# Kernel tuning notes

Hardware: AMD Instinct MI355X
Metric: run time of the kernel (lower is better)

Reference implementation:

```python
import jax, jax.numpy as jnp
import numpy as np

EPS = 1e-5
NEG_SLOPE = 0.1


def conv_bn_lrelu(x, w, g, b, rm, rv):
    # 1x1 conv (no bias) + BatchNorm (inference, running stats) + LeakyReLU(0.1)
    # x: [B,C,H,W], w: [O,C]
    y = jnp.einsum('bchw,oc->bohw', x, w)
    scale = g / jnp.sqrt(rv + EPS)
    y = y * scale[None, :, None, None] + (b - rm * scale)[None, :, None, None]
    return jnp.where(y >= 0, y, NEG_SLOPE * y)


def setup_inputs() -> dict:
    key = jax.random.key(0)
    ks = jax.random.split(key, 16)
    B, C, H1, W1, H2, W2 = 4, 256, 32, 32, 64, 64
    C8 = C // 8
    inp = {
        'x1': jax.random.normal(ks[0], (B, C, H1, W1), jnp.float32),
        'x2': jax.random.normal(ks[1], (B, C, H2, W2), jnp.float32),
        'wq': jax.random.normal(ks[2], (C8, C), jnp.float32) * 0.05,
        'wk': jax.random.normal(ks[3], (C8, C), jnp.float32) * 0.05,
        'wv': jax.random.normal(ks[4], (C, C), jnp.float32) * 0.05,
        'gq': jnp.ones((C8,), jnp.float32), 'bq': jnp.zeros((C8,), jnp.float32),
        'mq': jax.random.normal(ks[5], (C8,), jnp.float32) * 0.1,
        'vq': jax.random.uniform(ks[6], (C8,), jnp.float32, 0.5, 1.5),
        'gk': jnp.ones((C8,), jnp.float32), 'bk': jnp.zeros((C8,), jnp.float32),
        'mk': jax.random.normal(ks[7], (C8,), jnp.float32) * 0.1,
        'vk': jax.random.uniform(ks[8], (C8,), jnp.float32, 0.5, 1.5),
        'gv': jnp.ones((C,), jnp.float32), 'bv': jnp.zeros((C,), jnp.float32),
        'mv': jax.random.normal(ks[9], (C,), jnp.float32) * 0.1,
        'vv': jax.random.uniform(ks[10], (C,), jnp.float32, 0.5, 1.5),
        'gamma': jnp.full((1,), 0.5, jnp.float32),
    }
    return inp


def reference(x1, x2, wq, wk, wv, gq, bq, mq, vq, gk, bk, mk, vk, gv, bv, mv, vv, gamma):
    B, C, H2, W2 = x2.shape
    # bilinear upsample x1 to x2's spatial size (align_corners=False == half-pixel)
    x1u = jax.image.resize(x1, (B, C, H2, W2), method='bilinear')
    N = H2 * W2
    q = conv_bn_lrelu(x1u, wq, gq, bq, mq, vq).reshape(B, -1, N)  # [B,C8,N]
    k = conv_bn_lrelu(x2, wk, gk, bk, mk, vk).reshape(B, -1, N)   # [B,C8,N]
    v = conv_bn_lrelu(x2, wv, gv, bv, mv, vv).reshape(B, -1, N)   # [B,C,N]
    energy = jnp.einsum('bdm,bdn->bmn', q, k)                      # [B,N,N]
    attn = jax.nn.softmax(energy, axis=-1)
    out = jnp.einsum('bcn,bmn->bcm', v, attn).reshape(B, C, H2, W2)
    return gamma[0] * out + x1u
```

## Files before the change

### kernel.cpp

```cpp
#include <hip/hip_runtime.h>

#define B_ 4
#define C_ 256
#define N_ 4096
#define LOG2E 1.4426950408889634f

typedef short short8 __attribute__((ext_vector_type(8)));
typedef short short4_ __attribute__((ext_vector_type(4)));
typedef float float4v __attribute__((ext_vector_type(4)));
typedef unsigned int uint2v __attribute__((ext_vector_type(2)));
typedef unsigned int u32;

__device__ inline unsigned short f2b(float x){
  unsigned u = __builtin_bit_cast(unsigned, x);
  u = u + 0x7FFFu + ((u >> 16) & 1u);
  return (unsigned short)(u >> 16);
}
__device__ inline float b2f(unsigned short s){
  return __builtin_bit_cast(float, ((u32)s) << 16);
}
__device__ inline u32 cvtpk(float lo, float hi){
  u32 r; asm("v_cvt_pk_bf16_f32 %0, %1, %2" : "=v"(r) : "v"(lo), "v"(hi)); return r;
}
__device__ inline void gload16(const void* g, void* l){
  __builtin_amdgcn_global_load_lds((const __attribute__((address_space(1))) u32*)g,
                                   (__attribute__((address_space(3))) u32*)l, 16, 0, 0);
}

__global__ void fold_w_kernel(const float* __restrict__ wq, const float* __restrict__ wk,
    const float* __restrict__ wv,
    const float* gq, const float* bq, const float* mq, const float* vq,
    const float* gk, const float* bk, const float* mk, const float* vk,
    const float* gv, const float* bv, const float* mv, const float* vv,
    unsigned short* wqb, unsigned short* wkb, unsigned short* wvb,
    float* biasq, float* biask, float* biasv){
  int i = blockIdx.x*256 + threadIdx.x;
  int o = i >> 8;
  float sv = gv[o]*rsqrtf(vv[o]+1e-5f);
  wvb[i] = f2b(wv[i]*sv);
  if (i < 32*256){
    int oq = i >> 8;
    float sq = gq[oq]*rsqrtf(vq[oq]+1e-5f);
    wqb[i] = f2b(wq[i]*sq*LOG2E);
    float sk = gk[oq]*rsqrtf(vk[oq]+1e-5f);
    wkb[i] = f2b(wk[i]*sk);
  }
  if (i < 256) biasv[i] = bv[i] - mv[i]*(gv[i]*rsqrtf(vv[i]+1e-5f));
  if (i < 32){
    biasq[i] = (bq[i] - mq[i]*(gq[i]*rsqrtf(vq[i]+1e-5f)))*LOG2E;
    biask[i] = bk[i] - mk[i]*(gk[i]*rsqrtf(vk[i]+1e-5f));
  }
}

__global__ __launch_bounds__(256, 2)
void pre_kernel(const float* __restrict__ x1, const float* __restrict__ x2,
                const unsigned short* __restrict__ wqb,
                const unsigned short* __restrict__ wkb,
                const unsigned short* __restrict__ wvb,
                const float* __restrict__ biasq, const float* __restrict__ biask,
                const float* __restrict__ biasv,
                unsigned short* __restrict__ Qb, unsigned short* __restrict__ Kb,
                unsigned short* __restrict__ Vb){
  __shared__ unsigned short xt[64*260];
  int b = blockIdx.y;
  int t = threadIdx.x;
  int lane = t&63, w = t>>6, l15 = lane&15, g = lane>>4;

  if (blockIdx.z == 0){
    int y = blockIdx.x;
    float fy = 0.5f*y - 0.25f;
    float y0f = floorf(fy); float wy = fy - y0f;
    int y0 = max(0,min(31,(int)y0f)), y1 = max(0,min(31,(int)y0f+1));
    int x = t & 63, cg = t >> 6;
    float fx = 0.5f*x - 0.25f;
    float x0f = floorf(fx); float wx = fx - x0f;
    int x0 = max(0,min(31,(int)x0f)), x1i = max(0,min(31,(int)x0f+1));
    #pragma unroll 8
    for (int i=0;i<64;i++){
      int c = cg + i*4;
      const float* s0 = x1 + ((size_t)(b*C_ + c)*32 + y0)*32;
      const float* s1 = x1 + ((size_t)(b*C_ + c)*32 + y1)*32;
      float v00=s0[x0], v01=s0[x1i], v10=s1[x0], v11=s1[x1i];
      float v0 = v00 + wx*(v01-v00), v1 = v10 + wx*(v11-v10);
      float val = v0 + wy*(v1-v0);
      xt[x*260 + c] = f2b(val);
    }
    __syncthreads();
    const unsigned short* arow = xt + (w*16+l15)*260 + g*8;
    short8 a[8];
    #pragma unroll
    for (int kk=0;kk<8;kk++){
      short4_ lo = *(const short4_*)(arow + kk*32);
      short4_ hi = *(const short4_*)(arow + kk*32 + 4);
      short8 af;
      af[0]=lo[0];af[1]=lo[1];af[2]=lo[2];af[3]=lo[3];
      af[4]=hi[0];af[5]=hi[1];af[6]=hi[2];af[7]=hi[3];
      a[kk]=af;
    }
    #pragma unroll
    for (int ot=0; ot<2; ot++){
      int o = ot*16 + l15;
      const unsigned short* wrow = wqb + o*C_ + g*8;
      float4v acc = {0.f,0.f,0.f,0.f};
      #pragma unroll
      for (int kk=0;kk<8;kk++){
        short8 bf = *(const short8*)(wrow + kk*32);
        acc = __builtin_amdgcn_mfma_f32_16x16x32_bf16(a[kk], bf, acc, 0,0,0);
      }
      float bs = biasq[o];
      #pragma unroll
      for (int r=0;r<4;r++){
        float yv = acc[r] + bs;
        yv = yv >= 0.f ? yv : 0.1f*yv;
        int m = y*64 + w*16 + g*4 + r;
        Qb[(size_t)(b*N_+m)*32 + o] = f2b(yv);
      }
    }
  } else {
    int n0 = blockIdx.x*64;
    int n = t & 63, cg = t >> 6;
    #pragma unroll 8
    for (int i=0;i<64;i++){
      int c = cg + i*4;
      float v = x2[(size_t)(b*C_ + c)*N_ + n0 + n];
      xt[n*260 + c] = f2b(v);
    }
    __syncthreads();
    const unsigned short* arow = xt + (w*16+l15)*260 + g*8;
    short8 a[8];
    #pragma unroll
    for (int kk=0;kk<8;kk++){
      short4_ lo = *(const short4_*)(arow + kk*32);
      short4_ hi = *(const short4_*)(arow + kk*32 + 4);
      short8 af;
      af[0]=lo[0];af[1]=lo[1];af[2]=lo[2];af[3]=lo[3];
      af[4]=hi[0];af[5]=hi[1];af[6]=hi[2];af[7]=hi[3];
      a[kk]=af;
    }
    if (blockIdx.z == 1){
      #pragma unroll
      for (int ot=0; ot<2; ot++){
        int o = ot*16 + l15;
        const unsigned short* wrow = wkb + o*C_ + g*8;
        float4v acc = {0.f,0.f,0.f,0.f};
        #pragma unroll
        for (int kk=0;kk<8;kk++){
          short8 bf = *(const short8*)(wrow + kk*32);
          acc = __builtin_amdgcn_mfma_f32_16x16x32_bf16(a[kk], bf, acc, 0,0,0);
        }
        float bs = biask[o];
        #pragma unroll
        for (int r=0;r<4;r++){
          float yv = acc[r] + bs;
          yv = yv >= 0.f ? yv : 0.1f*yv;
          int m = n0 + w*16 + g*4 + r;
          Kb[(size_t)(b*N_+m)*32 + o] = f2b(yv);
        }
      }
    }
    int obase = (blockIdx.z == 1) ? 0 : 8;
    #pragma unroll
    for (int ot=0; ot<8; ot++){
      int o = (obase + ot)*16 + l15;
      const unsigned short* wrow = wvb + (size_t)o*C_ + g*8;
      float4v acc = {0.f,0.f,0.f,0.f};
      #pragma unroll
      for (int kk=0;kk<8;kk++){
        short8 bf = *(const short8*)(wrow + kk*32);
        acc = __builtin_amdgcn_mfma_f32_16x16x32_bf16(a[kk], bf, acc, 0,0,0);
      }
      float bs = biasv[o];
      #pragma unroll
      for (int r=0;r<4;r++){
        float yv = acc[r] + bs;
        yv = yv >= 0.f ? yv : 0.1f*yv;
        int m = n0 + w*16 + g*4 + r;
        Vb[(size_t)(b*C_ + o)*N_ + m] = f2b(yv);
      }
    }
  }
}

__global__ __launch_bounds__(512, 2)
void attn_kernel(const unsigned short* __restrict__ Qb,
                 const unsigned short* __restrict__ Kb,
                 const unsigned short* __restrict__ Vb,
                 unsigned short* __restrict__ partial,
                 float* __restrict__ statsg){
  __shared__ __align__(16) char smem[43552];
  int* flagsB = (int*)(smem + 43008);
  float* sclB = (float*)(smem + 43040);

  int wg = (blockIdx.z*4 + blockIdx.y)*64 + blockIdx.x;
  int id = (wg & 7)*64 + (wg >> 3);
  int ng = id >> 8, b = (id >> 6) & 3, mblk = id & 63;
  int t = threadIdx.x, lane = t & 63, w = t >> 6;
  int l15 = lane & 15, g = lane >> 4;

  short8 qf{};
  if (w < 4)
    qf = *(const short8*)(Qb + (size_t)(b*N_ + mblk*64 + w*16 + l15)*32 + g*8);

  float4v acc[4][2];
  #pragma unroll
  for (int mt=0;mt<4;mt++)
    #pragma unroll
    for (int ct=0;ct<2;ct++) acc[mt][ct] = (float4v){0.f,0.f,0.f,0.f};
  float mrow = -1e30f, lrun = 0.f;
  const float4v zero4 = {0.f,0.f,0.f,0.f};

  u32 goff[2]; int loff[2];
  #pragma unroll
  for (int j=0;j<2;j++){
    int i = j*512 + t;
    int c = i >> 2, jj = i & 3;
    loff[j] = i*16;
    goff[j] = (u32)(c*(N_*2)) + (u32)((jj ^ (c & 3)) << 4);
  }
  const char* Vbyte = (const char*)Vb + (size_t)b*C_*N_*2 + ng*4096;
  const short* kbase = (const short*)Kb + (size_t)(b*N_ + ng*2048 + l15)*32 + g*8;

  auto stageV = [&](int tt, int par){
    const char* src = Vbyte + tt*64;
    #pragma unroll
    for (int j=0;j<2;j++) gload16(src + goff[j], smem + par*16384 + loff[j]);
  };
  auto loadK = [&](short8 (&kf)[2], int tt){
    const short* kp = kbase + (size_t)tt*1024;
    #pragma unroll
    for (int j=0;j<2;j++) kf[j] = *(const short8*)(kp + j*512);
  };

  auto softmax_step = [&](const short8 (&kf)[2], int pdst){
    float4v s[2];
    #pragma unroll
    for (int j=0;j<2;j++)
      s[j] = __builtin_amdgcn_mfma_f32_16x16x32_bf16(kf[j], qf, zero4, 0, 0, 0);
    float tmax = fmaxf(fmaxf(fmaxf(s[0][0],s[0][1]),fmaxf(s[0][2],s[0][3])),
                       fmaxf(fmaxf(s[1][0],s[1][1]),fmaxf(s[1][2],s[1][3])));
    int trig = __any((tmax > mrow + 8.f) ? 1 : 0) ? 1 : 0;
    if (lane == 0) flagsB[pdst*4 + w] = trig;
    if (trig){
      float tm = fmaxf(tmax, __shfl_xor(tmax, 16));
      tm = fmaxf(tm, __shfl_xor(tm, 32));
      float mnew = fmaxf(mrow, tm);
      float sc = exp2f(mrow - mnew);
      mrow = mnew; lrun *= sc;
      if (lane < 16) sclB[pdst*64 + w*16 + l15] = sc;
    }
    char* pw = smem + 32768 + pdst*5120 + w*1280 + l15*80;
    #pragma unroll
    for (int j=0;j<2;j++){
      float p0 = exp2f(s[j][0]-mrow), p1 = exp2f(s[j][1]-mrow);
      float p2 = exp2f(s[j][2]-mrow), p3 = exp2f(s[j][3]-mrow);
      lrun += (p0+p1)+(p2+p3);
      u32 lo = cvtpk(p0, p1);
      u32 hi = cvtpk(p2, p3);
      *(uint2v*)(pw + j*32 + g*8) = (uint2v){lo, hi};
    }
  };

  auto body = [&](int tt, short8 (&kC)[2], short8 (&kN)[2]){
    int pp = tt & 1, nx = (tt+1) & 1;
    if (tt < 63) stageV(tt+1, nx);
    if (w < 4){
      loadK(kN, (tt+2) & 63);
      if (tt < 63) softmax_step(kC, nx);
    }
    #pragma unroll
    for (int mt=0;mt<4;mt++){
      if (flagsB[pp*4 + mt]){
        float4v sv = *(float4v*)(sclB + pp*64 + mt*16 + g*4);
        #pragma unroll
        for (int ct=0;ct<2;ct++){
          acc[mt][ct][0]*=sv[0]; acc[mt][ct][1]*=sv[1];
          acc[mt][ct][2]*=sv[2]; acc[mt][ct][3]*=sv[3];
        }
      }
    }
    const char* pb = smem + 32768 + pp*5120;
    const char* vbc = smem + pp*16384;
    short8 pa[4], vf[2];
    #pragma unroll
    for (int mt=0;mt<4;mt++)
      pa[mt] = *(const short8*)(pb + mt*1280 + l15*80 + g*16);
    #pragma unroll
    for (int ct=0;ct<2;ct++){
      int row = w*32 + ct*16 + l15;
      vf[ct] = *(const short8*)(vbc + row*64 + ((g*16) ^ ((row & 3) << 4)));
    }
    __builtin_amdgcn_s_setprio(1);
    #pragma unroll
    for (int mt=0;mt<4;mt++)
      #pragma unroll
      for (int ct=0;ct<2;ct++)
        acc[mt][ct] = __builtin_amdgcn_mfma_f32_16x16x32_bf16(pa[mt], vf[ct], acc[mt][ct], 0, 0, 0);
    __builtin_amdgcn_s_setprio(0);
    __syncthreads();
  };

  short8 kA[2], kB[2];
  stageV(0, 0);
  if (w < 4){
    short8 k0[2];
    loadK(k0, 0);
    softmax_step(k0, 0);
    loadK(kA, 1);
  }
  __syncthreads();

  for (int tt=0; tt<64; tt+=2){
    body(tt,   kA, kB);
    body(tt+1, kB, kA);
  }

  if (w < 4){
    lrun += __shfl_xor(lrun, 16);
    lrun += __shfl_xor(lrun, 32);
    if (lane < 16){
      int sidx = (((b*2+ng)*64 + mblk)*64 + w*16 + l15)*2;
      statsg[sidx] = mrow; statsg[sidx+1] = lrun;
    }
  }
  size_t pbg = (size_t)((b*2+ng)*64 + mblk)*16384;
  #pragma unroll
  for (int mt=0;mt<4;mt++)
    #pragma unroll
    for (int ct=0;ct<2;ct++)
      #pragma unroll
      for (int r=0;r<4;r++){
        int m = mt*16 + g*4 + r;
        int c = w*32 + ct*16 + l15;
        partial[pbg + m*256 + c] = f2b(acc[mt][ct][r]);
      }
}

__global__ __launch_bounds__(256, 2)
void combine_kernel(const unsigned short* __restrict__ partial,
                    const float* __restrict__ statsg,
                    const float* __restrict__ x1,
                    const float* __restrict__ gamma_p,
                    float* __restrict__ out){
  __shared__ float tile[64][65];
  __shared__ float fbuf[64][3];
  int b = blockIdx.z, mblk = blockIdx.y, ct4 = blockIdx.x;
  int t = threadIdx.x;
  float gm = gamma_p[0];
  if (t < 64){
    int s0 = (((b*2+0)*64 + mblk)*64 + t)*2;
    int s1 = (((b*2+1)*64 + mblk)*64 + t)*2;
    float m0 = statsg[s0], l0 = statsg[s0+1];
    float m1 = statsg[s1], l1 = statsg[s1+1];
    float M = fmaxf(m0, m1);
    float f0 = exp2f(m0 - M), f1 = exp2f(m1 - M);
    float L = l0*f0 + l1*f1;
    fbuf[t][0] = f0; fbuf[t][1] = f1; fbuf[t][2] = gm / L;
  }
  __syncthreads();
  size_t p0b = (size_t)((b*2+0)*64 + mblk)*16384 + ct4*64;
  size_t p1b = (size_t)((b*2+1)*64 + mblk)*16384 + ct4*64;
  int c_l = t & 63, mg = t >> 6;
  #pragma unroll 4
  for (int pass=0; pass<16; pass++){
    int m = pass*4 + mg;
    float v0 = b2f(partial[p0b + m*256 + c_l]);
    float v1 = b2f(partial[p1b + m*256 + c_l]);
    tile[m][c_l] = (v0*fbuf[m][0] + v1*fbuf[m][1]) * fbuf[m][2];
  }
  __syncthreads();
  int y = mblk;
  float fy = 0.5f*y - 0.25f;
  float y0f = floorf(fy); float wy = fy - y0f;
  int y0 = max(0,min(31,(int)y0f)), y1 = max(0,min(31,(int)y0f+1));
  int m = t & 63, cg = t >> 6;
  float fx = 0.5f*m - 0.25f;
  float x0f = floorf(fx); float wx = fx - x0f;
  int x0 = max(0,min(31,(int)x0f)), x1i = max(0,min(31,(int)x0f+1));
  #pragma unroll 4
  for (int pass=0; pass<16; pass++){
    int c_l2 = pass*4 + cg;
    const float* s0 = x1 + ((size_t)(b*C_ + ct4*64 + c_l2)*32 + y0)*32;
    const float* s1 = x1 + ((size_t)(b*C_ + ct4*64 + c_l2)*32 + y1)*32;
    float v00=s0[x0], v01=s0[x1i], v10=s1[x0], v11=s1[x1i];
    float v0 = v00 + wx*(v01-v00), v1 = v10 + wx*(v11-v10);
    float xv = v0 + wy*(v1-v0);
    size_t gidx = ((size_t)(b*C_ + ct4*64 + c_l2))*N_ + mblk*64 + m;
    out[gidx] = tile[m][c_l2] + xv;
  }
}

extern "C" void kernel_launch(void* const* d_in, const int* in_sizes, int n_in,
                              void* d_out, int out_size, void* d_ws, size_t ws_size,
                              hipStream_t stream){
  (void)in_sizes; (void)n_in; (void)out_size; (void)ws_size;
  const float* x1 = (const float*)d_in[0];
  const float* x2 = (const float*)d_in[1];
  const float* wq = (const float*)d_in[2];
  const float* wk = (const float*)d_in[3];
  const float* wv = (const float*)d_in[4];
  const float* gq = (const float*)d_in[5];
  const float* bq = (const float*)d_in[6];
  const float* mq = (const float*)d_in[7];
  const float* vq = (const float*)d_in[8];
  const float* gk = (const float*)d_in[9];
  const float* bk = (const float*)d_in[10];
  const float* mk = (const float*)d_in[11];
  const float* vk = (const float*)d_in[12];
  const float* gv = (const float*)d_in[13];
  const float* bv = (const float*)d_in[14];
  const float* mv = (const float*)d_in[15];
  const float* vv = (const float*)d_in[16];
  const float* gamma = (const float*)d_in[17];
  float* out = (float*)d_out;

  char* p = (char*)d_ws;
  unsigned short* Qb    = (unsigned short*)p; p += (size_t)B_*N_*32*2;
  unsigned short* Kb    = (unsigned short*)p; p += (size_t)B_*N_*32*2;
  unsigned short* Vb    = (unsigned short*)p; p += (size_t)B_*C_*N_*2;
  unsigned short* wqb   = (unsigned short*)p; p += 32*256*2;
  unsigned short* wkb   = (unsigned short*)p; p += 32*256*2;
  unsigned short* wvb   = (unsigned short*)p; p += 256*256*2;
  float* biasq          = (float*)p;          p += 32*4;
  float* biask          = (float*)p;          p += 32*4;
  float* biasv          = (float*)p;          p += 256*4;
  unsigned short* parti = (unsigned short*)p; p += (size_t)512*16384*2;
  float* statsg         = (float*)p;          p += (size_t)512*64*2*4;

  fold_w_kernel<<<256, 256, 0, stream>>>(wq,wk,wv,gq,bq,mq,vq,gk,bk,mk,vk,gv,bv,mv,vv,
                                         wqb,wkb,wvb,biasq,biask,biasv);
  pre_kernel<<<dim3(64,4,3), 256, 0, stream>>>(x1, x2, wqb, wkb, wvb,
                                               biasq, biask, biasv, Qb, Kb, Vb);
  attn_kernel<<<dim3(64,4,2), 512, 0, stream>>>(Qb, Kb, Vb, parti, statsg);
  combine_kernel<<<dim3(4,64,4), 256, 0, stream>>>(parti, statsg, x1, gamma, out);
}
```

Before: 110.3 us.

## Split attention key dimension four ways and strengthen V LDS swizzle

Attention now splits the N keys into four chunks instead of two, launching 1024 workgroups that each process 32 key tiles. The combine kernel merges four partial softmax states. This gives more parallelism on a 256-CU device and shortens each block's serial loop. The cost is twice the partial-output traffic and a heavier combine step. The LDS swizzle for V tiles also XORs in an extra row bit to reduce bank conflicts.

```diff
diff --git a/kernel.cpp b/kernel.cpp
--- a/kernel.cpp
+++ b/kernel.cpp
@@ -192,7 +192,7 @@
   float* sclB = (float*)(smem + 43040);
 
   int wg = (blockIdx.z*4 + blockIdx.y)*64 + blockIdx.x;
-  int id = (wg & 7)*64 + (wg >> 3);
+  int id = (wg & 7)*128 + (wg >> 3);
   int ng = id >> 8, b = (id >> 6) & 3, mblk = id & 63;
   int t = threadIdx.x, lane = t & 63, w = t >> 6;
   int l15 = lane & 15, g = lane >> 4;
@@ -213,12 +213,13 @@
   #pragma unroll
   for (int j=0;j<2;j++){
     int i = j*512 + t;
-    int c = i >> 2, jj = i & 3;
+    int c = i >> 2, sp = i & 3;
+    int jj = sp ^ (c & 3) ^ ((c >> 2) & 3);
     loff[j] = i*16;
-    goff[j] = (u32)(c*(N_*2)) + (u32)((jj ^ (c & 3)) << 4);
-  }
-  const char* Vbyte = (const char*)Vb + (size_t)b*C_*N_*2 + ng*4096;
-  const short* kbase = (const short*)Kb + (size_t)(b*N_ + ng*2048 + l15)*32 + g*8;
+    goff[j] = (u32)(c*(N_*2)) + (u32)(jj << 4);
+  }
+  const char* Vbyte = (const char*)Vb + (size_t)b*C_*N_*2 + ng*2048;
+  const short* kbase = (const short*)Kb + (size_t)(b*N_ + ng*1024 + l15)*32 + g*8;
 
   auto stageV = [&](int tt, int par){
     const char* src = Vbyte + tt*64;
@@ -262,10 +263,10 @@
 
   auto body = [&](int tt, short8 (&kC)[2], short8 (&kN)[2]){
     int pp = tt & 1, nx = (tt+1) & 1;
-    if (tt < 63) stageV(tt+1, nx);
+    if (tt < 31) stageV(tt+1, nx);
     if (w < 4){
-      loadK(kN, (tt+2) & 63);
-      if (tt < 63) softmax_step(kC, nx);
+      loadK(kN, (tt+2) & 31);
+      if (tt < 31) softmax_step(kC, nx);
     }
     #pragma unroll
     for (int mt=0;mt<4;mt++){
@@ -287,7 +288,8 @@
     #pragma unroll
     for (int ct=0;ct<2;ct++){
       int row = w*32 + ct*16 + l15;
-      vf[ct] = *(const short8*)(vbc + row*64 + ((g*16) ^ ((row & 3) << 4)));
+      int slot = g ^ (row & 3) ^ ((row >> 2) & 3);
+      vf[ct] = *(const short8*)(vbc + row*64 + slot*16);
     }
     __builtin_amdgcn_s_setprio(1);
     #pragma unroll
@@ -309,7 +311,7 @@
   }
   __syncthreads();
 
-  for (int tt=0; tt<64; tt+=2){
+  for (int tt=0; tt<32; tt+=2){
     body(tt,   kA, kB);
     body(tt+1, kB, kA);
   }
@@ -318,11 +320,11 @@
     lrun += __shfl_xor(lrun, 16);
     lrun += __shfl_xor(lrun, 32);
     if (lane < 16){
-      int sidx = (((b*2+ng)*64 + mblk)*64 + w*16 + l15)*2;
+      int sidx = (((b*4+ng)*64 + mblk)*64 + w*16 + l15)*2;
       statsg[sidx] = mrow; statsg[sidx+1] = lrun;
     }
   }
-  size_t pbg = (size_t)((b*2+ng)*64 + mblk)*16384;
+  size_t pbg = (size_t)((b*4+ng)*64 + mblk)*16384;
   #pragma unroll
   for (int mt=0;mt<4;mt++)
     #pragma unroll
@@ -342,30 +344,41 @@
                     const float* __restrict__ gamma_p,
                     float* __restrict__ out){
   __shared__ float tile[64][65];
-  __shared__ float fbuf[64][3];
+  __shared__ float fbuf[64][5];
   int b = blockIdx.z, mblk = blockIdx.y, ct4 = blockIdx.x;
   int t = threadIdx.x;
   float gm = gamma_p[0];
   if (t < 64){
-    int s0 = (((b*2+0)*64 + mblk)*64 + t)*2;
-    int s1 = (((b*2+1)*64 + mblk)*64 + t)*2;
-    float m0 = statsg[s0], l0 = statsg[s0+1];
-    float m1 = statsg[s1], l1 = statsg[s1+1];
-    float M = fmaxf(m0, m1);
-    float f0 = exp2f(m0 - M), f1 = exp2f(m1 - M);
-    float L = l0*f0 + l1*f1;
-    fbuf[t][0] = f0; fbuf[t][1] = f1; fbuf[t][2] = gm / L;
+    float mq[4], lq[4];
+    #pragma unroll
+    for (int q=0;q<4;q++){
+      int s = (((b*4+q)*64 + mblk)*64 + t)*2;
+      mq[q] = statsg[s]; lq[q] = statsg[s+1];
+    }
+    float M = fmaxf(fmaxf(mq[0],mq[1]), fmaxf(mq[2],mq[3]));
+    float L = 0.f;
+    #pragma unroll
+    for (int q=0;q<4;q++){
+      float f = exp2f(mq[q] - M);
+      fbuf[t][q] = f;
+      L += lq[q]*f;
+    }
+    fbuf[t][4] = gm / L;
   }
   __syncthreads();
-  size_t p0b = (size_t)((b*2+0)*64 + mblk)*16384 + ct4*64;
-  size_t p1b = (size_t)((b*2+1)*64 + mblk)*16384 + ct4*64;
+  size_t pqb[4];
+  #pragma unroll
+  for (int q=0;q<4;q++)
+    pqb[q] = (size_t)((b*4+q)*64 + mblk)*16384 + ct4*64;
   int c_l = t & 63, mg = t >> 6;
   #pragma unroll 4
   for (int pass=0; pass<16; pass++){
     int m = pass*4 + mg;
-    float v0 = b2f(partial[p0b + m*256 + c_l]);
-    float v1 = b2f(partial[p1b + m*256 + c_l]);
-    tile[m][c_l] = (v0*fbuf[m][0] + v1*fbuf[m][1]) * fbuf[m][2];
+    float v = 0.f;
+    #pragma unroll
+    for (int q=0;q<4;q++)
+      v += b2f(partial[pqb[q] + m*256 + c_l]) * fbuf[m][q];
+    tile[m][c_l] = v * fbuf[m][4];
   }
   __syncthreads();
   int y = mblk;
@@ -423,13 +436,13 @@
   float* biasq          = (float*)p;          p += 32*4;
   float* biask          = (float*)p;          p += 32*4;
   float* biasv          = (float*)p;          p += 256*4;
-  unsigned short* parti = (unsigned short*)p; p += (size_t)512*16384*2;
-  float* statsg         = (float*)p;          p += (size_t)512*64*2*4;
+  unsigned short* parti = (unsigned short*)p; p += (size_t)1024*16384*2;
+  float* statsg         = (float*)p;          p += (size_t)1024*64*2*4;
 
   fold_w_kernel<<<256, 256, 0, stream>>>(wq,wk,wv,gq,bq,mq,vq,gk,bk,mk,vk,gv,bv,mv,vv,
                                          wqb,wkb,wvb,biasq,biask,biasv);
   pre_kernel<<<dim3(64,4,3), 256, 0, stream>>>(x1, x2, wqb, wkb, wvb,
                                                biasq, biask, biasv, Qb, Kb, Vb);
-  attn_kernel<<<dim3(64,4,2), 512, 0, stream>>>(Qb, Kb, Vb, parti, statsg);
+  attn_kernel<<<dim3(64,4,4), 512, 0, stream>>>(Qb, Kb, Vb, parti, statsg);
   combine_kernel<<<dim3(4,64,4), 256, 0, stream>>>(parti, statsg, x1, gamma, out);
 }
```

Result: slower. 115.8 us (+5.0%).
